# Kernel optimization log

Measured on AMD Instinct MI355X. Metric: run time of the kernel, lower is better.

The kernel has to match this reference:

```python
import jax, jax.numpy as jnp
import numpy as np


def setup_inputs() -> dict:
    key = jax.random.key(0)
    k1, k2, k3 = jax.random.split(key, 3)
    B, S, A, C = 128, 52, 5, 20
    predictions = jax.random.normal(k1, (B, A * (5 + C), S, S), dtype=jnp.float32)
    t = jax.random.uniform(k2, (B, S, S, A, 5 + C), dtype=jnp.float32)
    mask = (jax.random.uniform(k3, (B, S, S, A)) < 0.05).astype(jnp.float32)
    targets = t.at[..., 4].set(mask)
    anchors = jnp.array([[1.08, 1.19], [3.42, 4.41], [6.63, 11.38],
                         [9.42, 5.11], [16.62, 10.52]], dtype=jnp.float32)
    return {"predictions": predictions, "targets": targets, "anchors": anchors}


def _yolov2_loss(predictions, targets, anchors):
    B, pred_dim, S, _ = predictions.shape
    A = anchors.shape[0]
    C = pred_dim // A - 5
    # [B, A, 5+C, S, S] -> [B, S, S, A, 5+C]
    p = predictions.reshape(B, A, 5 + C, S, S).transpose(0, 3, 4, 1, 2)
    tx, ty, tw, th = p[..., 0], p[..., 1], p[..., 2], p[..., 3]
    conf_logits = p[..., 4]
    class_logits = p[..., 5:]

    gx, gy, gw, gh = targets[..., 0], targets[..., 1], targets[..., 2], targets[..., 3]
    obj_mask = targets[..., 4]
    class_target = targets[..., 5:]

    pred_cx = jax.nn.sigmoid(tx)
    pred_cy = jax.nn.sigmoid(ty)
    pred_w = jnp.exp(tw) * anchors[:, 0]  # broadcast over trailing A dim
    pred_h = jnp.exp(th) * anchors[:, 1]

    # grid offsets: dim 1 is i (row -> cy), dim 2 is j (col -> cx)
    jj = jnp.arange(S, dtype=jnp.float32)[None, None, :, None]
    ii = jnp.arange(S, dtype=jnp.float32)[None, :, None, None]
    cx_gt, cy_gt = gx + jj, gy + ii
    cx_pr, cy_pr = pred_cx + jj, pred_cy + ii

    # vectorized corner-form IoU (only used where obj_mask == 1)
    x1min, x1max = cx_gt - gw / 2, cx_gt + gw / 2
    y1min, y1max = cy_gt - gh / 2, cy_gt + gh / 2
    x2min, x2max = cx_pr - pred_w / 2, cx_pr + pred_w / 2
    y2min, y2max = cy_pr - pred_h / 2, cy_pr + pred_h / 2
    inter_w = jnp.clip(jnp.minimum(x1max, x2max) - jnp.maximum(x1min, x2min), 0.0)
    inter_h = jnp.clip(jnp.minimum(y1max, y2max) - jnp.maximum(y1min, y2min), 0.0)
    inter = inter_w * inter_h
    union = gw * gh + pred_w * pred_h - inter
    iou = jnp.where(union > 0, inter / union, 0.0)

    loss_xy = jnp.sum(obj_mask * (jnp.square(pred_cx - gx) + jnp.square(pred_cy - gy)))
    eps = 1e-6
    loss_wh = jnp.sum(obj_mask * (jnp.square(jnp.sqrt(pred_w + eps) - jnp.sqrt(gw + eps))
                                  + jnp.square(jnp.sqrt(pred_h + eps) - jnp.sqrt(gh + eps))))

    conf_pred = jax.nn.sigmoid(conf_logits)
    loss_obj = jnp.sum(obj_mask * jnp.square(iou - conf_pred))
    loss_noobj = jnp.sum((1.0 - obj_mask) * jnp.square(conf_pred))

    # BCE with logits: softplus(x) - x * t (stable via logaddexp)
    bce = jnp.logaddexp(0.0, class_logits) - class_logits * class_target
    loss_cls = jnp.sum(obj_mask[..., None] * bce)

    total = 5.0 * (loss_xy + loss_wh) + 5.0 * loss_obj + 0.5 * loss_noobj + loss_cls
    return total, loss_xy + loss_wh, loss_cls, loss_obj + loss_noobj


def reference(predictions, targets, anchors):
    # returns (total, coord, class, obj) matching the original dict values
    return _yolov2_loss(predictions, targets, anchors)
```

## Files before the change

kernel.cpp:

```cpp
#include <hip/hip_runtime.h>

#define SS 2704
#define NA 5
#define NC 20
#define NB 128
#define CELLS (NB * SS)
#define TILE 64
#define TPB 320
#define NTILE (CELLS / TILE)
#define TILE_F (TILE * 125)
#define TILE_V4 (TILE_F / 4)
#define RBLOCK 256

__device__ __forceinline__ float fast_sigmoid(float x) {
    return __builtin_amdgcn_rcpf(1.0f + __expf(-x));
}
__device__ __forceinline__ float fast_softplus(float x) {
    return fmaxf(x, 0.0f) + __logf(1.0f + __expf(-fabsf(x)));
}

__global__ __launch_bounds__(TPB) void yolo_main(
        const float* __restrict__ P,
        const float* __restrict__ T,
        const float* __restrict__ anch,
        float* __restrict__ partial) {
    __shared__ float lds[TILE_F];
    __shared__ float red[NA][4];

    int tile = blockIdx.x;

    const float4* src = (const float4*)(T + (size_t)tile * TILE_F);
    float4* dst = (float4*)lds;
    #pragma unroll
    for (int i = 0; i < 7; ++i) {
        int idx = threadIdx.x + i * TPB;
        if (idx < TILE_V4) dst[idx] = src[idx];
    }
    __syncthreads();

    int a    = threadIdx.x >> 6;
    int lane = threadIdx.x & 63;
    int cell = tile * TILE + lane;
    int b    = cell / SS;
    int ij   = cell - b * SS;

    const float* Pa = P + ((size_t)b * 125 + a * 25) * SS + ij;
    const float* Tl = lds + lane * 125 + a * 25;
    float aw  = anch[2 * a];
    float ahv = anch[2 * a + 1];

    float fl = Tl[4];
    float cp = fast_sigmoid(Pa[4 * SS]);

    float s_xywh = 0.0f, s_cls = 0.0f, s_obj = 0.0f, s_noobj = 0.0f;

    if (fl != 0.0f) {
        float tx = Pa[0], ty = Pa[SS], tw = Pa[2 * SS], th = Pa[3 * SS];
        float gx = Tl[0], gy = Tl[1], gw = Tl[2], gh = Tl[3];
        float cx = fast_sigmoid(tx), cy = fast_sigmoid(ty);
        float pw = __expf(tw) * aw;
        float ph = __expf(th) * ahv;
        float iw = fmaxf(fminf(gx + 0.5f * gw, cx + 0.5f * pw) -
                         fmaxf(gx - 0.5f * gw, cx - 0.5f * pw), 0.0f);
        float ih = fmaxf(fminf(gy + 0.5f * gh, cy + 0.5f * ph) -
                         fmaxf(gy - 0.5f * gh, cy - 0.5f * ph), 0.0f);
        float inter = iw * ih;
        float uni   = gw * gh + pw * ph - inter;
        float iou   = (uni > 0.0f) ? inter * __builtin_amdgcn_rcpf(uni) : 0.0f;

        float dx = cx - gx, dy = cy - gy;
        s_xywh += dx * dx + dy * dy;
        const float eps = 1e-6f;
        float dw = __fsqrt_rn(pw + eps) - __fsqrt_rn(gw + eps);
        float dh = __fsqrt_rn(ph + eps) - __fsqrt_rn(gh + eps);
        s_xywh += dw * dw + dh * dh;

        float dob = iou - cp;
        s_obj += dob * dob;

        #pragma unroll
        for (int k = 0; k < NC; ++k) {
            float l = Pa[(size_t)(5 + k) * SS];
            float t = Tl[5 + k];
            s_cls += fast_softplus(l) - l * t;
        }
    } else {
        s_noobj = cp * cp;
    }

    #pragma unroll
    for (int off = 32; off > 0; off >>= 1) {
        s_xywh  += __shfl_xor(s_xywh,  off, 64);
        s_cls   += __shfl_xor(s_cls,   off, 64);
        s_obj   += __shfl_xor(s_obj,   off, 64);
        s_noobj += __shfl_xor(s_noobj, off, 64);
    }
    if (lane == 0) {
        red[a][0] = s_xywh; red[a][1] = s_cls; red[a][2] = s_obj; red[a][3] = s_noobj;
    }
    __syncthreads();
    if (threadIdx.x == 0) {
        float r0 = 0, r1 = 0, r2 = 0, r3 = 0;
        #pragma unroll
        for (int w = 0; w < NA; ++w) {
            r0 += red[w][0]; r1 += red[w][1]; r2 += red[w][2]; r3 += red[w][3];
        }
        float* p = partial + (size_t)blockIdx.x * 4;
        p[0] = r0; p[1] = r1; p[2] = r2; p[3] = r3;
    }
}

__global__ __launch_bounds__(RBLOCK) void yolo_reduce(
        const float* __restrict__ partial, int n, float* __restrict__ out) {
    float v0 = 0.0f, v1 = 0.0f, v2 = 0.0f, v3 = 0.0f;
    for (int i = threadIdx.x; i < n; i += RBLOCK) {
        const float* p = partial + (size_t)i * 4;
        v0 += p[0]; v1 += p[1]; v2 += p[2]; v3 += p[3];
    }
    #pragma unroll
    for (int off = 32; off > 0; off >>= 1) {
        v0 += __shfl_xor(v0, off, 64);
        v1 += __shfl_xor(v1, off, 64);
        v2 += __shfl_xor(v2, off, 64);
        v3 += __shfl_xor(v3, off, 64);
    }
    __shared__ float red[4][4];
    int wid = threadIdx.x >> 6, lane = threadIdx.x & 63;
    if (lane == 0) {
        red[wid][0] = v0; red[wid][1] = v1; red[wid][2] = v2; red[wid][3] = v3;
    }
    __syncthreads();
    if (threadIdx.x == 0) {
        float xywh = 0, cls = 0, obj = 0, noobj = 0;
        #pragma unroll
        for (int q = 0; q < 4; ++q) {
            xywh += red[q][0]; cls += red[q][1]; obj += red[q][2]; noobj += red[q][3];
        }
        out[0] = 5.0f * xywh + 5.0f * obj + 0.5f * noobj + cls;
        out[1] = xywh;
        out[2] = cls;
        out[3] = obj + noobj;
    }
}

extern "C" void kernel_launch(void* const* d_in, const int* in_sizes, int n_in,
                              void* d_out, int out_size, void* d_ws, size_t ws_size,
                              hipStream_t stream) {
    const float* P = (const float*)d_in[0];
    const float* T = (const float*)d_in[1];
    const float* anch = (const float*)d_in[2];
    float* out = (float*)d_out;
    float* partial = (float*)d_ws;

    yolo_main<<<NTILE, TPB, 0, stream>>>(P, T, anch, partial);
    yolo_reduce<<<1, RBLOCK, 0, stream>>>(partial, NTILE, out);
}
```

Before: 65.58 us.

## Process four tiles per block with register-staged prefetch of next target tile

Each block now handles four consecutive 64-cell tiles instead of one. The next tile's target data is prefetched into registers while the current tile is computed from LDS, which overlaps global loads with compute. This also cuts the number of partial sums, and the reduce kernel is widened to 1024 threads. The cost is higher register pressure from the 7 float4 staging registers, an extra barrier per tile, and fewer blocks to hide latency.

```diff
diff --git a/kernel.cpp b/kernel.cpp
--- a/kernel.cpp
+++ b/kernel.cpp
@@ -8,9 +8,11 @@
 #define TILE 64
 #define TPB 320
 #define NTILE (CELLS / TILE)
+#define TPB_TILES 4
+#define NBLK (NTILE / TPB_TILES)
 #define TILE_F (TILE * 125)
 #define TILE_V4 (TILE_F / 4)
-#define RBLOCK 256
+#define RBLOCK 1024
 
 __device__ __forceinline__ float fast_sigmoid(float x) {
     return __builtin_amdgcn_rcpf(1.0f + __expf(-x));
@@ -27,65 +29,92 @@
     __shared__ float lds[TILE_F];
     __shared__ float red[NA][4];
 
-    int tile = blockIdx.x;
-
-    const float4* src = (const float4*)(T + (size_t)tile * TILE_F);
-    float4* dst = (float4*)lds;
-    #pragma unroll
-    for (int i = 0; i < 7; ++i) {
-        int idx = threadIdx.x + i * TPB;
-        if (idx < TILE_V4) dst[idx] = src[idx];
-    }
-    __syncthreads();
-
     int a    = threadIdx.x >> 6;
     int lane = threadIdx.x & 63;
-    int cell = tile * TILE + lane;
-    int b    = cell / SS;
-    int ij   = cell - b * SS;
-
-    const float* Pa = P + ((size_t)b * 125 + a * 25) * SS + ij;
-    const float* Tl = lds + lane * 125 + a * 25;
     float aw  = anch[2 * a];
     float ahv = anch[2 * a + 1];
 
-    float fl = Tl[4];
-    float cp = fast_sigmoid(Pa[4 * SS]);
+    int tile0 = blockIdx.x * TPB_TILES;
+    int cell  = tile0 * TILE + lane;
+    int b     = cell / SS;
+    int ij    = cell - b * SS;
 
     float s_xywh = 0.0f, s_cls = 0.0f, s_obj = 0.0f, s_noobj = 0.0f;
 
-    if (fl != 0.0f) {
-        float tx = Pa[0], ty = Pa[SS], tw = Pa[2 * SS], th = Pa[3 * SS];
-        float gx = Tl[0], gy = Tl[1], gw = Tl[2], gh = Tl[3];
-        float cx = fast_sigmoid(tx), cy = fast_sigmoid(ty);
-        float pw = __expf(tw) * aw;
-        float ph = __expf(th) * ahv;
-        float iw = fmaxf(fminf(gx + 0.5f * gw, cx + 0.5f * pw) -
-                         fmaxf(gx - 0.5f * gw, cx - 0.5f * pw), 0.0f);
-        float ih = fmaxf(fminf(gy + 0.5f * gh, cy + 0.5f * ph) -
-                         fmaxf(gy - 0.5f * gh, cy - 0.5f * ph), 0.0f);
-        float inter = iw * ih;
-        float uni   = gw * gh + pw * ph - inter;
-        float iou   = (uni > 0.0f) ? inter * __builtin_amdgcn_rcpf(uni) : 0.0f;
+    float4 stg[7];
+    {
+        const float4* src = (const float4*)(T + (size_t)tile0 * TILE_F);
+        #pragma unroll
+        for (int i = 0; i < 7; ++i) {
+            int idx = threadIdx.x + i * TPB;
+            if (idx < TILE_V4) stg[i] = src[idx];
+        }
+    }
 
-        float dx = cx - gx, dy = cy - gy;
-        s_xywh += dx * dx + dy * dy;
-        const float eps = 1e-6f;
-        float dw = __fsqrt_rn(pw + eps) - __fsqrt_rn(gw + eps);
-        float dh = __fsqrt_rn(ph + eps) - __fsqrt_rn(gh + eps);
-        s_xywh += dw * dw + dh * dh;
+    for (int k = 0; k < TPB_TILES; ++k) {
+        {
+            float4* dst = (float4*)lds;
+            #pragma unroll
+            for (int i = 0; i < 7; ++i) {
+                int idx = threadIdx.x + i * TPB;
+                if (idx < TILE_V4) dst[idx] = stg[i];
+            }
+        }
+        __syncthreads();
 
-        float dob = iou - cp;
-        s_obj += dob * dob;
+        if (k + 1 < TPB_TILES) {
+            const float4* src = (const float4*)(T + (size_t)(tile0 + k + 1) * TILE_F);
+            #pragma unroll
+            for (int i = 0; i < 7; ++i) {
+                int idx = threadIdx.x + i * TPB;
+                if (idx < TILE_V4) stg[i] = src[idx];
+            }
+        }
 
-        #pragma unroll
-        for (int k = 0; k < NC; ++k) {
-            float l = Pa[(size_t)(5 + k) * SS];
-            float t = Tl[5 + k];
-            s_cls += fast_softplus(l) - l * t;
+        const float* Pa = P + ((size_t)b * 125 + a * 25) * SS + ij;
+        const float* Tl = lds + lane * 125 + a * 25;
+
+        float fl = Tl[4];
+        float cp = fast_sigmoid(Pa[4 * SS]);
+
+        if (fl != 0.0f) {
+            float tx = Pa[0], ty = Pa[SS], tw = Pa[2 * SS], th = Pa[3 * SS];
+            float gx = Tl[0], gy = Tl[1], gw = Tl[2], gh = Tl[3];
+            float cx = fast_sigmoid(tx), cy = fast_sigmoid(ty);
+            float pw = __expf(tw) * aw;
+            float ph = __expf(th) * ahv;
+            float iw = fmaxf(fminf(gx + 0.5f * gw, cx + 0.5f * pw) -
+                             fmaxf(gx - 0.5f * gw, cx - 0.5f * pw), 0.0f);
+            float ih = fmaxf(fminf(gy + 0.5f * gh, cy + 0.5f * ph) -
+                             fmaxf(gy - 0.5f * gh, cy - 0.5f * ph), 0.0f);
+            float inter = iw * ih;
+            float uni   = gw * gh + pw * ph - inter;
+            float iou   = (uni > 0.0f) ? inter * __builtin_amdgcn_rcpf(uni) : 0.0f;
+
+            float dx = cx - gx, dy = cy - gy;
+            s_xywh += dx * dx + dy * dy;
+            const float eps = 1e-6f;
+            float dw = __fsqrt_rn(pw + eps) - __fsqrt_rn(gw + eps);
+            float dh = __fsqrt_rn(ph + eps) - __fsqrt_rn(gh + eps);
+            s_xywh += dw * dw + dh * dh;
+
+            float dob = iou - cp;
+            s_obj += dob * dob;
+
+            #pragma unroll
+            for (int c = 0; c < NC; ++c) {
+                float l = Pa[(size_t)(5 + c) * SS];
+                float t = Tl[5 + c];
+                s_cls += fast_softplus(l) - l * t;
+            }
+        } else {
+            s_noobj += cp * cp;
         }
-    } else {
-        s_noobj = cp * cp;
+
+        __syncthreads();
+
+        ij += TILE;
+        if (ij >= SS) { ij -= SS; b += 1; }
     }
 
     #pragma unroll
@@ -124,7 +153,7 @@
         v2 += __shfl_xor(v2, off, 64);
         v3 += __shfl_xor(v3, off, 64);
     }
-    __shared__ float red[4][4];
+    __shared__ float red[16][4];
     int wid = threadIdx.x >> 6, lane = threadIdx.x & 63;
     if (lane == 0) {
         red[wid][0] = v0; red[wid][1] = v1; red[wid][2] = v2; red[wid][3] = v3;
@@ -133,7 +162,7 @@
     if (threadIdx.x == 0) {
         float xywh = 0, cls = 0, obj = 0, noobj = 0;
         #pragma unroll
-        for (int q = 0; q < 4; ++q) {
+        for (int q = 0; q < RBLOCK / 64; ++q) {
             xywh += red[q][0]; cls += red[q][1]; obj += red[q][2]; noobj += red[q][3];
         }
         out[0] = 5.0f * xywh + 5.0f * obj + 0.5f * noobj + cls;
@@ -152,6 +181,6 @@
     float* out = (float*)d_out;
     float* partial = (float*)d_ws;
 
-    yolo_main<<<NTILE, TPB, 0, stream>>>(P, T, anch, partial);
-    yolo_reduce<<<1, RBLOCK, 0, stream>>>(partial, NTILE, out);
+    yolo_main<<<NBLK, TPB, 0, stream>>>(P, T, anch, partial);
+    yolo_reduce<<<1, RBLOCK, 0, stream>>>(partial, NBLK, out);
 }
```

After: 125.6 us. +91.5%, slower.
